# Kernel optimization log

Measured on AMD Instinct MI355X. Metric: run time of the kernel, lower is better.

## Reference

```python
import jax, jax.numpy as jnp
import numpy as np

N, T = 20000, 32          # vertices, temporal depth
E = 640000                # edges (avg degree 32)
L = 2                     # number of SAGE layers
K, C, PAD = 5, 10, 2      # conv kernel size, out_channels, 'same' padding


def setup_inputs() -> dict:
    key = jax.random.key(0)
    ks = jax.random.split(key, 6)
    x = jax.random.normal(ks[0], (N, T), dtype=jnp.float32)
    edge_index = jax.random.randint(ks[1], (2, E), 0, N)
    # Conv1d(in_channels=1, out_channels=10, kernel_size=5) per layer -> [L, C, 1, K]
    convW = jax.random.normal(ks[2], (L, C, 1, K), dtype=jnp.float32) * 0.3
    convb = jax.random.normal(ks[3], (L, C), dtype=jnp.float32) * 0.1
    # GraphNorm params (initialized as in source: ones/ones/zeros)
    alpha = jnp.ones((L, T), dtype=jnp.float32)
    scale = jnp.ones((L, T), dtype=jnp.float32)
    shift = jnp.zeros((L, T), dtype=jnp.float32)
    # output Linear(in_features=N, out_features=3)
    Wout = jax.random.normal(ks[4], (3, N), dtype=jnp.float32) * (1.0 / np.sqrt(N))
    bout = jax.random.normal(ks[5], (3,), dtype=jnp.float32) * 0.01
    return dict(x=x, convW=convW, convb=convb, alpha=alpha, scale=scale,
                shift=shift, Wout=Wout, bout=bout, edge_index=edge_index)


def reference(x, convW, convb, alpha, scale, shift, Wout, bout, edge_index):
    src = edge_index[0]  # x_j gathered from source nodes
    dst = edge_index[1]  # aggregated at target nodes
    sqrt_n = jnp.sqrt(jnp.asarray(N, x.dtype))
    counts = jax.ops.segment_sum(jnp.ones((E,), x.dtype), dst, num_segments=N)
    denom = jnp.maximum(counts, 1.0)[:, None]  # mean aggr; isolated nodes -> 0
    for l in range(L):
        # GraphNorm
        x = x - alpha[l] * jnp.mean(x, axis=0)
        x = x / (jnp.linalg.norm(x, axis=0) / sqrt_n)
        x = x * scale[l] + shift[l]
        # message: gather + Conv1d(1->10, 'same') + max over channels
        xj = x[src][:, None, :]  # [E, 1, T]
        msg = jax.lax.conv_general_dilated(
            xj, convW[l], window_strides=(1,), padding=[(PAD, PAD)],
            dimension_numbers=('NCH', 'OIH', 'NCH'))  # [E, C, T]
        msg = jnp.max(msg + convb[l][None, :, None], axis=1)  # [E, T]
        # mean scatter-aggregate, then update + ReLU
        aggr = jax.ops.segment_sum(msg, dst, num_segments=N) / denom  # [N, T]
        x = jax.nn.relu(0.5 * (x + aggr))
    s = jnp.sum(x, axis=1)  # [N] sum over temporal dim
    return Wout @ s + bout   # [3] logits
```

## Files before the change

kernel.cpp:

```cpp
#include <hip/hip_runtime.h>
#include <hip/hip_bf16.h>

constexpr int N   = 20000;
constexpr int T   = 32;
constexpr int E   = 640000;
constexpr int C   = 10;
constexpr int K   = 5;
constexpr int SB  = 16;
constexpr int OB  = 64;
constexpr int NR  = 8;
constexpr int CAP = 80;
constexpr int RSPAN  = N / NR;
constexpr int ZWORDS = N + 2 * SB * 64 + OB * 3;

__global__ void k_zero(int* __restrict__ p) {
    int i = blockIdx.x * 256 + threadIdx.x;
    if (i < ZWORDS) p[i] = 0;
}

__global__ __launch_bounds__(256) void k_bin(
    const int* __restrict__ src, const int* __restrict__ dst,
    int* __restrict__ deg, unsigned short* __restrict__ slot,
    const float* __restrict__ x, float* __restrict__ statsA) {
    __shared__ float sred[64];
    int tid = threadIdx.x;
    int range   = blockIdx.x & (NR - 1);
    int chunk   = blockIdx.x >> 3;
    int nchunks = gridDim.x >> 3;
    int lo = range * RSPAN, hi = lo + RSPAN;
    int per = (E + nchunks - 1) / nchunks;
    int e0 = chunk * per;
    int e1 = e0 + per; if (e1 > E) e1 = E;
    for (int e = e0 + tid; e < e1; e += 256) {
        int d = dst[e];
        if (d >= lo && d < hi) {
            int p = atomicAdd(&deg[d], 1);
            if (p < CAP) slot[d * CAP + p] = (unsigned short)src[e];
        }
    }
    int gid = blockIdx.x * 256 + tid;
    int GS  = gridDim.x * 256;
    const float4* x4 = (const float4*)x;
    float s0 = 0.f, s1 = 0.f, s2 = 0.f, s3 = 0.f;
    float q0 = 0.f, q1 = 0.f, q2 = 0.f, q3 = 0.f;
    for (int i = gid; i < N * T / 4; i += GS) {
        float4 v = x4[i];
        s0 += v.x; q0 += v.x * v.x;
        s1 += v.y; q1 += v.y * v.y;
        s2 += v.z; q2 += v.z * v.z;
        s3 += v.w; q3 += v.w * v.w;
    }
    int c4 = (tid & 7) * 4;
#pragma unroll
    for (int ofs = 8; ofs < 64; ofs <<= 1) {
        s0 += __shfl_xor(s0, ofs); q0 += __shfl_xor(q0, ofs);
        s1 += __shfl_xor(s1, ofs); q1 += __shfl_xor(q1, ofs);
        s2 += __shfl_xor(s2, ofs); q2 += __shfl_xor(q2, ofs);
        s3 += __shfl_xor(s3, ofs); q3 += __shfl_xor(q3, ofs);
    }
    if (tid < 64) sred[tid] = 0.f;
    __syncthreads();
    if ((tid & 63) < 8) {
        atomicAdd(&sred[c4 + 0], s0); atomicAdd(&sred[32 + c4 + 0], q0);
        atomicAdd(&sred[c4 + 1], s1); atomicAdd(&sred[32 + c4 + 1], q1);
        atomicAdd(&sred[c4 + 2], s2); atomicAdd(&sred[32 + c4 + 2], q2);
        atomicAdd(&sred[c4 + 3], s3); atomicAdd(&sred[32 + c4 + 3], q3);
    }
    __syncthreads();
    if (tid < 64)
        atomicAdd(&statsA[(blockIdx.x & (SB - 1)) * 64 + tid], sred[tid]);
}

__global__ __launch_bounds__(256) void k_node(
    const float* __restrict__ xin, const float* __restrict__ grep,
    const float* __restrict__ Wl, const float* __restrict__ bl,
    const float* __restrict__ al, const float* __restrict__ sl,
    const float* __restrict__ shl,
    float* __restrict__ xhat, unsigned short* __restrict__ msg) {
    int gid = blockIdx.x * 256 + threadIdx.x;
    int t = gid & 31;
    int row = gid >> 5;
    if (row >= N) return;

    float Sx = 0.f, Sx2 = 0.f;
#pragma unroll
    for (int b = 0; b < SB; ++b) {
        Sx  += grep[b * 64 + t];
        Sx2 += grep[b * 64 + 32 + t];
    }
    float mu   = Sx * (1.0f / (float)N);
    float am   = al[t] * mu;
    float nrm2 = Sx2 - 2.f * am * Sx + (float)N * am * am;
    float g    = sl[t] * sqrtf((float)N) * rsqrtf(nrm2);
    float h    = shl[t] - am * g;

    float v = g * xin[row * T + t] + h;
    xhat[row * T + t] = v;
    float vm2 = __shfl(v, t - 2, 32); if (t < 2)  vm2 = 0.f;
    float vm1 = __shfl(v, t - 1, 32); if (t < 1)  vm1 = 0.f;
    float vp1 = __shfl(v, t + 1, 32); if (t > 30) vp1 = 0.f;
    float vp2 = __shfl(v, t + 2, 32); if (t > 29) vp2 = 0.f;
    float m = -3.0e38f;
#pragma unroll
    for (int c = 0; c < C; ++c) {
        float a = bl[c] + Wl[c * K + 0] * vm2 + Wl[c * K + 1] * vm1
                        + Wl[c * K + 2] * v   + Wl[c * K + 3] * vp1
                        + Wl[c * K + 4] * vp2;
        m = fmaxf(m, a);
    }
    __hip_bfloat16 mb = __float2bfloat16(m);
    msg[row * T + t] = *(unsigned short*)&mb;
}

__device__ __forceinline__ float gather_core(
    const int* __restrict__ deg, const unsigned short* __restrict__ slot,
    const unsigned short* __restrict__ msg, const float* __restrict__ xhat,
    int n, int t, int eo) {
    int dg  = deg[n];
    int cnt = dg < CAP ? dg : CAP;
    const unsigned short* sl = slot + n * CAP;
    float acc = 0.f;
    int i = eo;
    for (; i + 14 < cnt; i += 16) {
        int s0 = sl[i],      s1 = sl[i + 2],  s2 = sl[i + 4],  s3 = sl[i + 6];
        int s4 = sl[i + 8],  s5 = sl[i + 10], s6 = sl[i + 12], s7 = sl[i + 14];
        acc += __uint_as_float((unsigned)msg[s0 * T + t] << 16);
        acc += __uint_as_float((unsigned)msg[s1 * T + t] << 16);
        acc += __uint_as_float((unsigned)msg[s2 * T + t] << 16);
        acc += __uint_as_float((unsigned)msg[s3 * T + t] << 16);
        acc += __uint_as_float((unsigned)msg[s4 * T + t] << 16);
        acc += __uint_as_float((unsigned)msg[s5 * T + t] << 16);
        acc += __uint_as_float((unsigned)msg[s6 * T + t] << 16);
        acc += __uint_as_float((unsigned)msg[s7 * T + t] << 16);
    }
    for (; i < cnt; i += 2)
        acc += __uint_as_float((unsigned)msg[(int)sl[i] * T + t] << 16);
    acc += __shfl_xor(acc, 32);
    float r = 1.0f / fmaxf((float)dg, 1.0f);
    return fmaxf(0.5f * (xhat[n * T + t] + acc * r), 0.f);
}

__global__ __launch_bounds__(256) void k_gather0(
    const int* __restrict__ deg, const unsigned short* __restrict__ slot,
    const unsigned short* __restrict__ msg, const float* __restrict__ xhat,
    float* __restrict__ xout, float* __restrict__ statsB) {
    __shared__ float sred[64];
    int tid  = threadIdx.x;
    int gid  = blockIdx.x * 256 + tid;
    int lane = tid & 63;
    int t = lane & 31, eo = lane >> 5;
    int n = gid >> 6;

    float sx = 0.f, sx2 = 0.f;
    if (n < N) {
        float v = gather_core(deg, slot, msg, xhat, n, t, eo);
        if (eo == 0) {
            xout[n * T + t] = v;
            sx = v; sx2 = v * v;
        }
    }
    sx  += __shfl_xor(sx, 32);
    sx2 += __shfl_xor(sx2, 32);
    if (tid < 64) sred[tid] = 0.f;
    __syncthreads();
    if ((tid & 63) < 32) {
        atomicAdd(&sred[t], sx);
        atomicAdd(&sred[32 + t], sx2);
    }
    __syncthreads();
    if (tid < 64)
        atomicAdd(&statsB[(blockIdx.x & (SB - 1)) * 64 + tid], sred[tid]);
}

__global__ __launch_bounds__(256) void k_gather1(
    const int* __restrict__ deg, const unsigned short* __restrict__ slot,
    const unsigned short* __restrict__ msg, const float* __restrict__ xhat,
    const float* __restrict__ Wout, float* __restrict__ opart) {
    __shared__ float sred[3];
    int tid  = threadIdx.x;
    int gid  = blockIdx.x * 256 + tid;
    int lane = tid & 63;
    int t = lane & 31, eo = lane >> 5;
    int n = gid >> 6;

    float v = 0.f;
    if (n < N) v = gather_core(deg, slot, msg, xhat, n, t, eo);

    float s = (eo == 0) ? v : 0.f;
    s += __shfl_xor(s, 16); s += __shfl_xor(s, 8);
    s += __shfl_xor(s, 4);  s += __shfl_xor(s, 2); s += __shfl_xor(s, 1);
    float pa0 = 0.f, pa1 = 0.f, pa2 = 0.f;
    if (n < N && lane == 0) {
        pa0 = Wout[n] * s;
        pa1 = Wout[N + n] * s;
        pa2 = Wout[2 * N + n] * s;
    }
    if (tid < 3) sred[tid] = 0.f;
    __syncthreads();
    if (lane == 0) {
        atomicAdd(&sred[0], pa0);
        atomicAdd(&sred[1], pa1);
        atomicAdd(&sred[2], pa2);
    }
    __syncthreads();
    if (tid < 3)
        atomicAdd(&opart[(blockIdx.x & (OB - 1)) * 3 + tid], sred[tid]);
}

__global__ void k_finout(const float* __restrict__ opart,
                         const float* __restrict__ bout,
                         float* __restrict__ out) {
    int j = threadIdx.x;
    if (j < 3) {
        float s = bout[j];
        for (int b = 0; b < OB; ++b) s += opart[b * 3 + j];
        out[j] = s;
    }
}

extern "C" void kernel_launch(void* const* d_in, const int* in_sizes, int n_in,
                              void* d_out, int out_size, void* d_ws, size_t ws_size,
                              hipStream_t stream) {
    const float* x     = (const float*)d_in[0];
    const float* convW = (const float*)d_in[1];
    const float* convb = (const float*)d_in[2];
    const float* alpha = (const float*)d_in[3];
    const float* scale = (const float*)d_in[4];
    const float* shift = (const float*)d_in[5];
    const float* Wout  = (const float*)d_in[6];
    const float* bout  = (const float*)d_in[7];
    const int*   ei    = (const int*)d_in[8];
    const int* src = ei;
    const int* dst = ei + E;

    int*            deg    = (int*)d_ws;
    float*          statsA = (float*)(deg + N);
    float*          statsB = statsA + SB * 64;
    float*          opart  = statsB + SB * 64;
    unsigned short* slot   = (unsigned short*)(opart + OB * 3);
    unsigned short* msg    = slot + (size_t)N * CAP;
    float*          xhat   = (float*)(msg + (size_t)N * T);
    float*          x1     = xhat + N * T;
    float*          out    = (float*)d_out;

    k_zero<<<(ZWORDS + 255) / 256, 256, 0, stream>>>(deg);

    k_bin<<<2048, 256, 0, stream>>>(src, dst, deg, slot, x, statsA);

    k_node<<<(N * 32 + 255) / 256, 256, 0, stream>>>(
        x, statsA, convW, convb, alpha, scale, shift, xhat, msg);

    k_gather0<<<(N * 64 + 255) / 256, 256, 0, stream>>>(
        deg, slot, msg, xhat, x1, statsB);

    k_node<<<(N * 32 + 255) / 256, 256, 0, stream>>>(
        x1, statsB, convW + C * K, convb + C,
        alpha + T, scale + T, shift + T, xhat, msg);

    k_gather1<<<(N * 64 + 255) / 256, 256, 0, stream>>>(
        deg, slot, msg, xhat, Wout, opart);

    k_finout<<<1, 64, 0, stream>>>(opart, bout, out);
}
```

Baseline: 104.3 us.

## Gather packed bf16 pairs with four edge groups per node and unroll binning

The gather kernels now assign 16 lanes per node row. Each lane loads a 32-bit word holding two bf16 timesteps, and four edge-stride groups are reduced with shuffles. Before, 32 lanes each loaded 16-bit values across two groups. This halves the number of load instructions and widens each memory access. The binning loop is unrolled 4x to keep more independent dst loads and atomics in flight. CAP rises from 80 to 96, which lowers the chance of dropping edges for high-degree nodes at the cost of a larger slot array.

```diff
diff --git a/kernel.cpp b/kernel.cpp
--- a/kernel.cpp
+++ b/kernel.cpp
@@ -9,9 +9,16 @@
 constexpr int SB  = 16;
 constexpr int OB  = 64;
 constexpr int NR  = 8;
-constexpr int CAP = 80;
+constexpr int CAP = 96;
 constexpr int RSPAN  = N / NR;
 constexpr int ZWORDS = N + 2 * SB * 64 + OB * 3;
+
+__device__ __forceinline__ float bf_lo(unsigned m) {
+    return __uint_as_float(m << 16);
+}
+__device__ __forceinline__ float bf_hi(unsigned m) {
+    return __uint_as_float(m & 0xffff0000u);
+}
 
 __global__ void k_zero(int* __restrict__ p) {
     int i = blockIdx.x * 256 + threadIdx.x;
@@ -31,7 +38,27 @@
     int per = (E + nchunks - 1) / nchunks;
     int e0 = chunk * per;
     int e1 = e0 + per; if (e1 > E) e1 = E;
-    for (int e = e0 + tid; e < e1; e += 256) {
+    int e = e0 + tid;
+    for (; e + 768 < e1; e += 1024) {
+        int d0 = dst[e], d1 = dst[e + 256], d2 = dst[e + 512], d3 = dst[e + 768];
+        if (d0 >= lo && d0 < hi) {
+            int p = atomicAdd(&deg[d0], 1);
+            if (p < CAP) slot[d0 * CAP + p] = (unsigned short)src[e];
+        }
+        if (d1 >= lo && d1 < hi) {
+            int p = atomicAdd(&deg[d1], 1);
+            if (p < CAP) slot[d1 * CAP + p] = (unsigned short)src[e + 256];
+        }
+        if (d2 >= lo && d2 < hi) {
+            int p = atomicAdd(&deg[d2], 1);
+            if (p < CAP) slot[d2 * CAP + p] = (unsigned short)src[e + 512];
+        }
+        if (d3 >= lo && d3 < hi) {
+            int p = atomicAdd(&deg[d3], 1);
+            if (p < CAP) slot[d3 * CAP + p] = (unsigned short)src[e + 768];
+        }
+    }
+    for (; e < e1; e += 256) {
         int d = dst[e];
         if (d >= lo && d < hi) {
             int p = atomicAdd(&deg[d], 1);
@@ -112,60 +139,65 @@
     msg[row * T + t] = *(unsigned short*)&mb;
 }
 
-__device__ __forceinline__ float gather_core(
+__device__ __forceinline__ void gather_core(
     const int* __restrict__ deg, const unsigned short* __restrict__ slot,
-    const unsigned short* __restrict__ msg, const float* __restrict__ xhat,
-    int n, int t, int eo) {
+    const unsigned* __restrict__ msgp, const float* __restrict__ xhat,
+    int n, int c, int g, float* v0out, float* v1out) {
     int dg  = deg[n];
     int cnt = dg < CAP ? dg : CAP;
     const unsigned short* sl = slot + n * CAP;
-    float acc = 0.f;
-    int i = eo;
-    for (; i + 14 < cnt; i += 16) {
-        int s0 = sl[i],      s1 = sl[i + 2],  s2 = sl[i + 4],  s3 = sl[i + 6];
-        int s4 = sl[i + 8],  s5 = sl[i + 10], s6 = sl[i + 12], s7 = sl[i + 14];
-        acc += __uint_as_float((unsigned)msg[s0 * T + t] << 16);
-        acc += __uint_as_float((unsigned)msg[s1 * T + t] << 16);
-        acc += __uint_as_float((unsigned)msg[s2 * T + t] << 16);
-        acc += __uint_as_float((unsigned)msg[s3 * T + t] << 16);
-        acc += __uint_as_float((unsigned)msg[s4 * T + t] << 16);
-        acc += __uint_as_float((unsigned)msg[s5 * T + t] << 16);
-        acc += __uint_as_float((unsigned)msg[s6 * T + t] << 16);
-        acc += __uint_as_float((unsigned)msg[s7 * T + t] << 16);
-    }
-    for (; i < cnt; i += 2)
-        acc += __uint_as_float((unsigned)msg[(int)sl[i] * T + t] << 16);
-    acc += __shfl_xor(acc, 32);
+    float a0 = 0.f, a1 = 0.f;
+    int i = g;
+    for (; i + 12 < cnt; i += 16) {
+        int s0 = sl[i], s1 = sl[i + 4], s2 = sl[i + 8], s3 = sl[i + 12];
+        unsigned m0 = msgp[s0 * 16 + c];
+        unsigned m1 = msgp[s1 * 16 + c];
+        unsigned m2 = msgp[s2 * 16 + c];
+        unsigned m3 = msgp[s3 * 16 + c];
+        a0 += bf_lo(m0); a1 += bf_hi(m0);
+        a0 += bf_lo(m1); a1 += bf_hi(m1);
+        a0 += bf_lo(m2); a1 += bf_hi(m2);
+        a0 += bf_lo(m3); a1 += bf_hi(m3);
+    }
+    for (; i < cnt; i += 4) {
+        unsigned m = msgp[(int)sl[i] * 16 + c];
+        a0 += bf_lo(m); a1 += bf_hi(m);
+    }
+    a0 += __shfl_xor(a0, 16); a0 += __shfl_xor(a0, 32);
+    a1 += __shfl_xor(a1, 16); a1 += __shfl_xor(a1, 32);
     float r = 1.0f / fmaxf((float)dg, 1.0f);
-    return fmaxf(0.5f * (xhat[n * T + t] + acc * r), 0.f);
+    float2 xh = ((const float2*)(xhat + n * T))[c];
+    *v0out = fmaxf(0.5f * (xh.x + a0 * r), 0.f);
+    *v1out = fmaxf(0.5f * (xh.y + a1 * r), 0.f);
 }
 
 __global__ __launch_bounds__(256) void k_gather0(
     const int* __restrict__ deg, const unsigned short* __restrict__ slot,
-    const unsigned short* __restrict__ msg, const float* __restrict__ xhat,
+    const unsigned* __restrict__ msgp, const float* __restrict__ xhat,
     float* __restrict__ xout, float* __restrict__ statsB) {
     __shared__ float sred[64];
     int tid  = threadIdx.x;
     int gid  = blockIdx.x * 256 + tid;
     int lane = tid & 63;
-    int t = lane & 31, eo = lane >> 5;
+    int g = lane >> 4, c = lane & 15;
     int n = gid >> 6;
 
-    float sx = 0.f, sx2 = 0.f;
-    if (n < N) {
-        float v = gather_core(deg, slot, msg, xhat, n, t, eo);
-        if (eo == 0) {
-            xout[n * T + t] = v;
-            sx = v; sx2 = v * v;
-        }
-    }
-    sx  += __shfl_xor(sx, 32);
-    sx2 += __shfl_xor(sx2, 32);
+    float v0 = 0.f, v1 = 0.f;
+    bool valid = (n < N);
+    if (valid) {
+        gather_core(deg, slot, msgp, xhat, n, c, g, &v0, &v1);
+        if (g == 0) {
+            float2 w; w.x = v0; w.y = v1;
+            ((float2*)(xout + n * T))[c] = w;
+        }
+    }
     if (tid < 64) sred[tid] = 0.f;
     __syncthreads();
-    if ((tid & 63) < 32) {
-        atomicAdd(&sred[t], sx);
-        atomicAdd(&sred[32 + t], sx2);
+    if (valid && g == 0) {
+        atomicAdd(&sred[2 * c],          v0);
+        atomicAdd(&sred[2 * c + 1],      v1);
+        atomicAdd(&sred[32 + 2 * c],     v0 * v0);
+        atomicAdd(&sred[32 + 2 * c + 1], v1 * v1);
     }
     __syncthreads();
     if (tid < 64)
@@ -174,23 +206,24 @@
 
 __global__ __launch_bounds__(256) void k_gather1(
     const int* __restrict__ deg, const unsigned short* __restrict__ slot,
-    const unsigned short* __restrict__ msg, const float* __restrict__ xhat,
+    const unsigned* __restrict__ msgp, const float* __restrict__ xhat,
     const float* __restrict__ Wout, float* __restrict__ opart) {
     __shared__ float sred[3];
     int tid  = threadIdx.x;
     int gid  = blockIdx.x * 256 + tid;
     int lane = tid & 63;
-    int t = lane & 31, eo = lane >> 5;
+    int g = lane >> 4, c = lane & 15;
     int n = gid >> 6;
 
-    float v = 0.f;
-    if (n < N) v = gather_core(deg, slot, msg, xhat, n, t, eo);
-
-    float s = (eo == 0) ? v : 0.f;
-    s += __shfl_xor(s, 16); s += __shfl_xor(s, 8);
-    s += __shfl_xor(s, 4);  s += __shfl_xor(s, 2); s += __shfl_xor(s, 1);
+    float v0 = 0.f, v1 = 0.f;
+    bool valid = (n < N);
+    if (valid) gather_core(deg, slot, msgp, xhat, n, c, g, &v0, &v1);
+
+    float s = v0 + v1;
+    s += __shfl_xor(s, 1); s += __shfl_xor(s, 2);
+    s += __shfl_xor(s, 4); s += __shfl_xor(s, 8);
     float pa0 = 0.f, pa1 = 0.f, pa2 = 0.f;
-    if (n < N && lane == 0) {
+    if (valid && lane == 0) {
         pa0 = Wout[n] * s;
         pa1 = Wout[N + n] * s;
         pa2 = Wout[2 * N + n] * s;
@@ -251,14 +284,14 @@
         x, statsA, convW, convb, alpha, scale, shift, xhat, msg);
 
     k_gather0<<<(N * 64 + 255) / 256, 256, 0, stream>>>(
-        deg, slot, msg, xhat, x1, statsB);
+        deg, slot, (const unsigned*)msg, xhat, x1, statsB);
 
     k_node<<<(N * 32 + 255) / 256, 256, 0, stream>>>(
         x1, statsB, convW + C * K, convb + C,
         alpha + T, scale + T, shift + T, xhat, msg);
 
     k_gather1<<<(N * 64 + 255) / 256, 256, 0, stream>>>(
-        deg, slot, msg, xhat, Wout, opart);
+        deg, slot, (const unsigned*)msg, xhat, Wout, opart);
 
     k_finout<<<1, 64, 0, stream>>>(opart, bout, out);
 }
```

Result: faster. 98.74 us (-5.3%).
